# Kernel optimization log

Hardware: AMD Instinct MI355X
Metric: run time of the kernel (lower is better)

## Reference

```python
import jax, jax.numpy as jnp
import numpy as np

N_NODES = 50000
N_EDGES = 50000  # per-node attention scores are used as per-hyperedge weights => M == N
IN_CH = 128
OUT_CH = 128
NNZ = 800000


def setup_inputs() -> dict:
    key = jax.random.key(0)
    k = jax.random.split(key, 7)
    x = jax.random.normal(k[0], (N_NODES, IN_CH), dtype=jnp.float32)
    node_idx = jax.random.randint(k[1], (NNZ,), 0, N_NODES)
    edge_idx = jax.random.randint(k[2], (NNZ,), 0, N_EDGES)
    hyperedge_index = jnp.stack([node_idx, edge_idx]).astype(jnp.int64)
    s_in = 1.0 / np.sqrt(IN_CH)
    attn_w = jax.random.uniform(k[3], (1, IN_CH), minval=-s_in, maxval=s_in, dtype=jnp.float32)
    attn_b = jax.random.uniform(k[4], (1,), minval=-s_in, maxval=s_in, dtype=jnp.float32)
    lin_w = jax.random.uniform(k[5], (OUT_CH, IN_CH), minval=-s_in, maxval=s_in, dtype=jnp.float32)
    bias = jax.random.uniform(k[6], (OUT_CH,), minval=-s_in, maxval=s_in, dtype=jnp.float32)
    return {"x": x, "hyperedge_index": hyperedge_index,
            "attn_w": attn_w, "attn_b": attn_b, "lin_w": lin_w, "bias": bias}


def reference(x, hyperedge_index, attn_w, attn_b, lin_w, bias):
    # x: [N, C_in]; hyperedge_index: [2, nnz] (row 0: node ids, row 1: hyperedge ids)
    node_idx = hyperedge_index[0]
    edge_idx = hyperedge_index[1]
    N = x.shape[0]
    M = N_EDGES

    # edge_weight = sigmoid(attn(x)) -> used as hyperedge_weight (per-edge, M == N)
    w = jax.nn.sigmoid(x @ attn_w.T + attn_b)[:, 0]            # [M]

    xl = x @ lin_w.T                                           # [N, C_out]

    # D_v = sum of incident hyperedge weights per node; D^{-1} with inf -> 0
    D = jax.ops.segment_sum(w[edge_idx], node_idx, num_segments=N)
    Dinv = jnp.where(D > 0, 1.0 / D, 0.0)                      # [N]

    # B_e = hyperedge degree; B^{-1} with inf -> 0
    ones = jnp.ones(edge_idx.shape, dtype=x.dtype)
    Bdeg = jax.ops.segment_sum(ones, edge_idx, num_segments=M)
    Binv = jnp.where(Bdeg > 0, 1.0 / Bdeg, 0.0)                # [M]

    # node -> hyperedge: message = B_e^{-1} * x_j, aggregated at edge e
    msg = Binv[edge_idx][:, None] * xl[node_idx]               # [nnz, C_out]
    e_feat = jax.ops.segment_sum(msg, edge_idx, num_segments=M)

    # hyperedge -> node: message = D_v^{-1} * e_feat, aggregated at node v
    out = jax.ops.segment_sum(e_feat[edge_idx], node_idx, num_segments=N)
    out = Dinv[:, None] * out

    return out + bias
```

## Files before the change

### kernel.cpp

```cpp
#include <hip/hip_runtime.h>
#include <math.h>

#define CH 128
#define CAP 64
#define RSB 9
#define RS  (1 << RSB)
#define CAPB 10240
#define PB 2048

typedef __attribute__((ext_vector_type(8))) short bf16x8;
typedef __attribute__((ext_vector_type(4))) float f32x4;

__device__ __forceinline__ unsigned short f2bf(float f) {
    union { float f; unsigned u; } v; v.f = f;
    unsigned r = v.u + 0x7FFF + ((v.u >> 16) & 1);
    return (unsigned short)(r >> 16);
}
__device__ __forceinline__ float bflo(unsigned u) {
    union { unsigned u; float f; } v; v.u = u << 16; return v.f;
}
__device__ __forceinline__ float bfhi(unsigned u) {
    union { unsigned u; float f; } v; v.u = u & 0xFFFF0000u; return v.f;
}
__device__ __forceinline__ unsigned pack2bf(float a, float b) {
    return (unsigned)f2bf(a) | ((unsigned)f2bf(b) << 16);
}

__global__ __launch_bounds__(256) void fused_main(const float* __restrict__ x,
                                                  const float* __restrict__ attn_w,
                                                  const float* __restrict__ attn_b,
                                                  const float* __restrict__ lw,
                                                  unsigned short* __restrict__ xl,
                                                  float* __restrict__ w,
                                                  int nStrips,
                                                  const int* __restrict__ nidx,
                                                  const int* __restrict__ eidx,
                                                  int* __restrict__ binCnt,
                                                  unsigned int* __restrict__ binData,
                                                  int nnz, int nbd, int SB) {
    __shared__ unsigned short wl[128 * 136];
    __shared__ float awl[128];
    if ((int)blockIdx.x < SB) {
        int* hist = (int*)wl;
        int* base = ((int*)wl) + 256;
        int nbt = 2 * nbd;
        for (int i = threadIdx.x; i < nbt; i += 256) hist[i] = 0;
        __syncthreads();
        int k0 = blockIdx.x * PB + threadIdx.x;
        int vv[8], ee[8], sE[8], sN[8];
#pragma unroll
        for (int u = 0; u < 8; ++u) {
            int k = k0 + u * 256;
            if (k < nnz) {
                int v = nidx[k], e = eidx[k];
                vv[u] = v; ee[u] = e;
                sE[u] = atomicAdd(&hist[e >> RSB], 1);
                sN[u] = atomicAdd(&hist[nbd + (v >> RSB)], 1);
            } else vv[u] = -1;
        }
        __syncthreads();
        for (int i = threadIdx.x; i < nbt; i += 256)
            base[i] = atomicAdd(&binCnt[i], hist[i]);
        __syncthreads();
#pragma unroll
        for (int u = 0; u < 8; ++u) {
            if (vv[u] < 0) continue;
            int bE = ee[u] >> RSB;
            int bN = nbd + (vv[u] >> RSB);
            int iE = min(base[bE] + sE[u], CAPB - 1);
            int iN = min(base[bN] + sN[u], CAPB - 1);
            binData[(size_t)bE * CAPB + iE] = ((unsigned)ee[u] << 16) | (unsigned)vv[u];
            binData[(size_t)bN * CAPB + iN] = ((unsigned)vv[u] << 16) | (unsigned)ee[u];
        }
        return;
    }
    int tid = threadIdx.x;
    for (int i = tid; i < 2048; i += 256) {
        float4 vlo = ((const float4*)lw)[2 * i];
        float4 vhi = ((const float4*)lw)[2 * i + 1];
        int4 dst;
        dst.x = (int)pack2bf(vlo.x, vlo.y);
        dst.y = (int)pack2bf(vlo.z, vlo.w);
        dst.z = (int)pack2bf(vhi.x, vhi.y);
        dst.w = (int)pack2bf(vhi.z, vhi.w);
        *(int4*)(wl + (i >> 4) * 136 + (i & 15) * 8) = dst;
    }
    if (tid < 128) awl[tid] = attn_w[tid];
    float ab = attn_b[0];
    __syncthreads();
    int gb = blockIdx.x - SB;
    int wid = (gb << 2) | (tid >> 6);
    int lane = tid & 63;
    int m = lane & 15, quad = lane >> 4;
    int nWaves = ((int)gridDim.x - SB) << 2;
    for (int s = wid; s < nStrips; s += nWaves) {
        int r0 = s << 4;
        const float* xr = x + (size_t)(r0 + m) * CH + quad * 8;
        float att = 0.f;
        bf16x8 a0, a1, a2, a3;
#define LOAD_FRAG(AFRAG, F)                                                   \
        {                                                                     \
            float4 lo = *(const float4*)(xr + (F) * 32);                      \
            float4 hi = *(const float4*)(xr + (F) * 32 + 4);                  \
            const float* ap = &awl[(F) * 32 + quad * 8];                      \
            att += lo.x * ap[0] + lo.y * ap[1] + lo.z * ap[2] + lo.w * ap[3]  \
                 + hi.x * ap[4] + hi.y * ap[5] + hi.z * ap[6] + hi.w * ap[7]; \
            union { int4 i; bf16x8 v; } pk;                                   \
            pk.i.x = (int)pack2bf(lo.x, lo.y);                                \
            pk.i.y = (int)pack2bf(lo.z, lo.w);                                \
            pk.i.z = (int)pack2bf(hi.x, hi.y);                                \
            pk.i.w = (int)pack2bf(hi.z, hi.w);                                \
            AFRAG = pk.v;                                                     \
        }
        LOAD_FRAG(a0, 0)
        LOAD_FRAG(a1, 1)
        LOAD_FRAG(a2, 2)
        LOAD_FRAG(a3, 3)
#undef LOAD_FRAG
        att += __shfl_xor(att, 16, 64);
        att += __shfl_xor(att, 32, 64);
        if (quad == 0) w[r0 + m] = 1.0f / (1.0f + expf(-(att + ab)));
        unsigned short* orow = xl + (size_t)(r0 + quad * 4) * CH + m;
#pragma unroll
        for (int c0 = 0; c0 < 128; c0 += 16) {
            const unsigned short* wr = wl + (c0 + m) * 136 + quad * 8;
            f32x4 acc = {0.f, 0.f, 0.f, 0.f};
            acc = __builtin_amdgcn_mfma_f32_16x16x32_bf16(a0, *(const bf16x8*)(wr), acc, 0, 0, 0);
            acc = __builtin_amdgcn_mfma_f32_16x16x32_bf16(a1, *(const bf16x8*)(wr + 32), acc, 0, 0, 0);
            acc = __builtin_amdgcn_mfma_f32_16x16x32_bf16(a2, *(const bf16x8*)(wr + 64), acc, 0, 0, 0);
            acc = __builtin_amdgcn_mfma_f32_16x16x32_bf16(a3, *(const bf16x8*)(wr + 96), acc, 0, 0, 0);
            orow[c0]            = f2bf(acc[0]);
            orow[c0 + CH]       = f2bf(acc[1]);
            orow[c0 + 2 * CH]   = f2bf(acc[2]);
            orow[c0 + 3 * CH]   = f2bf(acc[3]);
        }
    }
}

__global__ __launch_bounds__(256) void bucket_build(const int* __restrict__ binCnt,
                                                    const unsigned int* __restrict__ binData,
                                                    int* __restrict__ cntE,
                                                    unsigned short* __restrict__ colE,
                                                    int* __restrict__ cntN,
                                                    unsigned short* __restrict__ colN,
                                                    int nbd, int N) {
    __shared__ int cl[RS];
    int b = blockIdx.x;
    int isN = b >= nbd;
    int bl = isN ? b - nbd : b;
    int idBase = bl << RSB;
    int* cnt = isN ? cntN : cntE;
    unsigned short* col = isN ? colN : colE;
    for (int i = threadIdx.x; i < RS; i += 256) cl[i] = 0;
    __syncthreads();
    int n = min(binCnt[b], CAPB);
    const unsigned int* src = binData + (size_t)b * CAPB;
    for (int i = threadIdx.x; i < n; i += 256) {
        unsigned int entry = src[i];
        int id  = (int)(entry >> 16);
        int val = (int)(entry & 0xFFFFu);
        int r = atomicAdd(&cl[id - idBase], 1);
        col[(size_t)id * CAP + min(r, CAP - 1)] = (unsigned short)val;
    }
    __syncthreads();
    for (int i = threadIdx.x; i < RS; i += 256) {
        int gid = idBase + i;
        if (gid < N) cnt[gid] = cl[i];
    }
}

__global__ __launch_bounds__(256) void edge_pull(const int* __restrict__ cntE,
                                                 const unsigned short* __restrict__ colE,
                                                 const unsigned short* __restrict__ xl,
                                                 unsigned short* __restrict__ ef, int M) {
    int e = (blockIdx.x << 2) | (threadIdx.x >> 6);
    if (e >= M) return;
    int lane = threadIdx.x & 63;
    int deg = cntE[e];
    const unsigned short* col = colE + (size_t)e * CAP;
    float2 a0 = {0.f, 0.f}, a1 = {0.f, 0.f}, a2 = {0.f, 0.f}, a3 = {0.f, 0.f};
    int j = 0;
    for (; j + 3 < deg; j += 4) {
        int v0 = col[j], v1 = col[j + 1], v2 = col[j + 2], v3 = col[j + 3];
        unsigned u0 = *(const unsigned*)(xl + (size_t)v0 * CH + 2 * lane);
        unsigned u1 = *(const unsigned*)(xl + (size_t)v1 * CH + 2 * lane);
        unsigned u2 = *(const unsigned*)(xl + (size_t)v2 * CH + 2 * lane);
        unsigned u3 = *(const unsigned*)(xl + (size_t)v3 * CH + 2 * lane);
        a0.x += bflo(u0); a0.y += bfhi(u0);
        a1.x += bflo(u1); a1.y += bfhi(u1);
        a2.x += bflo(u2); a2.y += bfhi(u2);
        a3.x += bflo(u3); a3.y += bfhi(u3);
    }
    for (; j < deg; ++j) {
        unsigned u0 = *(const unsigned*)(xl + (size_t)col[j] * CH + 2 * lane);
        a0.x += bflo(u0); a0.y += bfhi(u0);
    }
    a0.x += a1.x + a2.x + a3.x;
    a0.y += a1.y + a2.y + a3.y;
    float binv = deg > 0 ? 1.0f / (float)deg : 0.0f;
    *(unsigned*)(ef + (size_t)e * CH + 2 * lane) = pack2bf(a0.x * binv, a0.y * binv);
}

__global__ __launch_bounds__(256) void node_pull(const int* __restrict__ cntN,
                                                 const unsigned short* __restrict__ colN,
                                                 const unsigned short* __restrict__ ef,
                                                 const float* __restrict__ w,
                                                 const float* __restrict__ bias,
                                                 float* __restrict__ out, int N) {
    int v = (blockIdx.x << 2) | (threadIdx.x >> 6);
    if (v >= N) return;
    int lane = threadIdx.x & 63;
    int deg = cntN[v];
    const unsigned short* col = colN + (size_t)v * CAP;
    float2 a0 = {0.f, 0.f}, a1 = {0.f, 0.f}, a2 = {0.f, 0.f}, a3 = {0.f, 0.f};
    float ds = 0.f;
    int j = 0;
    for (; j + 3 < deg; j += 4) {
        int e0 = col[j], e1 = col[j + 1], e2 = col[j + 2], e3 = col[j + 3];
        unsigned u0 = *(const unsigned*)(ef + (size_t)e0 * CH + 2 * lane);
        unsigned u1 = *(const unsigned*)(ef + (size_t)e1 * CH + 2 * lane);
        unsigned u2 = *(const unsigned*)(ef + (size_t)e2 * CH + 2 * lane);
        unsigned u3 = *(const unsigned*)(ef + (size_t)e3 * CH + 2 * lane);
        ds += w[e0] + w[e1] + w[e2] + w[e3];
        a0.x += bflo(u0); a0.y += bfhi(u0);
        a1.x += bflo(u1); a1.y += bfhi(u1);
        a2.x += bflo(u2); a2.y += bfhi(u2);
        a3.x += bflo(u3); a3.y += bfhi(u3);
    }
    for (; j < deg; ++j) {
        int e0 = col[j];
        unsigned u0 = *(const unsigned*)(ef + (size_t)e0 * CH + 2 * lane);
        ds += w[e0];
        a0.x += bflo(u0); a0.y += bfhi(u0);
    }
    a0.x += a1.x + a2.x + a3.x;
    a0.y += a1.y + a2.y + a3.y;
    float dinv = ds > 0.f ? 1.0f / ds : 0.0f;
    float2 bi = *(const float2*)(bias + 2 * lane);
    float2 o = {a0.x * dinv + bi.x, a0.y * dinv + bi.y};
    *(float2*)(out + (size_t)v * CH + 2 * lane) = o;
}

extern "C" void kernel_launch(void* const* d_in, const int* in_sizes, int n_in,
                              void* d_out, int out_size, void* d_ws, size_t ws_size,
                              hipStream_t stream) {
    const float* x      = (const float*)d_in[0];
    const int*   hei    = (const int*)d_in[1];
    const float* attn_w = (const float*)d_in[2];
    const float* attn_b = (const float*)d_in[3];
    const float* lin_w  = (const float*)d_in[4];
    const float* bias   = (const float*)d_in[5];
    float* out = (float*)d_out;

    const int N   = in_sizes[0] / CH;
    const int nnz = in_sizes[1] / 2;
    const int* nidx = hei;
    const int* eidx = hei + nnz;

    unsigned short* S    = (unsigned short*)d_ws;
    float*          w    = (float*)(S + (size_t)N * CH);
    int*            cntE = (int*)(w + N);
    int*            cntN = cntE + N;
    unsigned short* colE = (unsigned short*)(cntN + N);
    unsigned short* colN = colE + (size_t)N * CAP;

    unsigned int* binData = (unsigned int*)S;
    int*          binCnt  = (int*)((char*)d_ws + (size_t)12 * 1024 * 1024);
    unsigned short* efbf = S;
    unsigned short* xlbf = (unsigned short*)out;

    int nbd = (N + RS - 1) >> RSB;
    hipMemsetAsync(binCnt, 0, (size_t)2 * nbd * sizeof(int), stream);

    int SB = (nnz + PB - 1) / PB;
    int nStrips = N / 16;
    int GB = (nStrips + 3) / 4;
    fused_main<<<SB + GB, 256, 0, stream>>>(x, attn_w, attn_b, lin_w, xlbf, w,
                                            nStrips, nidx, eidx, binCnt, binData,
                                            nnz, nbd, SB);

    bucket_build<<<2 * nbd, 256, 0, stream>>>(binCnt, binData, cntE, colE, cntN, colN, nbd, N);
    edge_pull<<<(N + 3) / 4, 256, 0, stream>>>(cntE, colE, xlbf, efbf, N);
    node_pull<<<(N + 3) / 4, 256, 0, stream>>>(cntN, colN, efbf, w, bias, out, N);
}
```

Before: 197.2 us.

## Fuse bucket build into edge and node aggregation kernels via shared-memory buckets

Removes the separate bucket_build kernel and the global colE/colN adjacency arrays. Each aggregation block now rescans one coarse bin's entries, keeps the 64 ids that belong to its sub-range, and builds per-id neighbor lists in shared memory before gathering. This saves one launch and the global write and read-back of the adjacency lists. In exchange each coarse bin is read eight times, once per sub-block, and blocks grow to 512 threads with a 64x64 shared bucket. Bin count atomics are also skipped for empty histogram bins.

```diff
diff --git a/kernel.cpp b/kernel.cpp
--- a/kernel.cpp
+++ b/kernel.cpp
@@ -7,6 +7,8 @@
 #define RS  (1 << RSB)
 #define CAPB 10240
 #define PB 2048
+#define SUB 8
+#define IDS 64
 
 typedef __attribute__((ext_vector_type(8))) short bf16x8;
 typedef __attribute__((ext_vector_type(4))) float f32x4;
@@ -60,7 +62,7 @@
         }
         __syncthreads();
         for (int i = threadIdx.x; i < nbt; i += 256)
-            base[i] = atomicAdd(&binCnt[i], hist[i]);
+            if (hist[i]) base[i] = atomicAdd(&binCnt[i], hist[i]);
         __syncthreads();
 #pragma unroll
         for (int u = 0; u < 8; ++u) {
@@ -137,108 +139,118 @@
     }
 }
 
-__global__ __launch_bounds__(256) void bucket_build(const int* __restrict__ binCnt,
-                                                    const unsigned int* __restrict__ binData,
-                                                    int* __restrict__ cntE,
-                                                    unsigned short* __restrict__ colE,
-                                                    int* __restrict__ cntN,
-                                                    unsigned short* __restrict__ colN,
-                                                    int nbd, int N) {
-    __shared__ int cl[RS];
-    int b = blockIdx.x;
-    int isN = b >= nbd;
-    int bl = isN ? b - nbd : b;
-    int idBase = bl << RSB;
-    int* cnt = isN ? cntN : cntE;
-    unsigned short* col = isN ? colN : colE;
-    for (int i = threadIdx.x; i < RS; i += 256) cl[i] = 0;
-    __syncthreads();
-    int n = min(binCnt[b], CAPB);
-    const unsigned int* src = binData + (size_t)b * CAPB;
-    for (int i = threadIdx.x; i < n; i += 256) {
+__global__ __launch_bounds__(512) void edge_agg(const int* __restrict__ binCnt,
+                                                const unsigned int* __restrict__ binData,
+                                                const unsigned short* __restrict__ xl,
+                                                unsigned short* __restrict__ ef, int M) {
+    __shared__ unsigned short bucket[IDS * CAP];
+    __shared__ int cl[IDS];
+    int cb = blockIdx.x >> 3;
+    int sr = blockIdx.x & (SUB - 1);
+    int idBase = (cb << RSB) + (sr << 6);
+    for (int i = threadIdx.x; i < IDS; i += 512) cl[i] = 0;
+    __syncthreads();
+    int n = min(binCnt[cb], CAPB);
+    const unsigned int* src = binData + (size_t)cb * CAPB;
+    for (int i = threadIdx.x; i < n; i += 512) {
         unsigned int entry = src[i];
-        int id  = (int)(entry >> 16);
-        int val = (int)(entry & 0xFFFFu);
-        int r = atomicAdd(&cl[id - idBase], 1);
-        col[(size_t)id * CAP + min(r, CAP - 1)] = (unsigned short)val;
-    }
-    __syncthreads();
-    for (int i = threadIdx.x; i < RS; i += 256) {
-        int gid = idBase + i;
-        if (gid < N) cnt[gid] = cl[i];
-    }
-}
-
-__global__ __launch_bounds__(256) void edge_pull(const int* __restrict__ cntE,
-                                                 const unsigned short* __restrict__ colE,
-                                                 const unsigned short* __restrict__ xl,
-                                                 unsigned short* __restrict__ ef, int M) {
-    int e = (blockIdx.x << 2) | (threadIdx.x >> 6);
-    if (e >= M) return;
-    int lane = threadIdx.x & 63;
-    int deg = cntE[e];
-    const unsigned short* col = colE + (size_t)e * CAP;
-    float2 a0 = {0.f, 0.f}, a1 = {0.f, 0.f}, a2 = {0.f, 0.f}, a3 = {0.f, 0.f};
-    int j = 0;
-    for (; j + 3 < deg; j += 4) {
-        int v0 = col[j], v1 = col[j + 1], v2 = col[j + 2], v3 = col[j + 3];
-        unsigned u0 = *(const unsigned*)(xl + (size_t)v0 * CH + 2 * lane);
-        unsigned u1 = *(const unsigned*)(xl + (size_t)v1 * CH + 2 * lane);
-        unsigned u2 = *(const unsigned*)(xl + (size_t)v2 * CH + 2 * lane);
-        unsigned u3 = *(const unsigned*)(xl + (size_t)v3 * CH + 2 * lane);
-        a0.x += bflo(u0); a0.y += bfhi(u0);
-        a1.x += bflo(u1); a1.y += bfhi(u1);
-        a2.x += bflo(u2); a2.y += bfhi(u2);
-        a3.x += bflo(u3); a3.y += bfhi(u3);
-    }
-    for (; j < deg; ++j) {
-        unsigned u0 = *(const unsigned*)(xl + (size_t)col[j] * CH + 2 * lane);
-        a0.x += bflo(u0); a0.y += bfhi(u0);
-    }
-    a0.x += a1.x + a2.x + a3.x;
-    a0.y += a1.y + a2.y + a3.y;
-    float binv = deg > 0 ? 1.0f / (float)deg : 0.0f;
-    *(unsigned*)(ef + (size_t)e * CH + 2 * lane) = pack2bf(a0.x * binv, a0.y * binv);
-}
-
-__global__ __launch_bounds__(256) void node_pull(const int* __restrict__ cntN,
-                                                 const unsigned short* __restrict__ colN,
-                                                 const unsigned short* __restrict__ ef,
-                                                 const float* __restrict__ w,
-                                                 const float* __restrict__ bias,
-                                                 float* __restrict__ out, int N) {
-    int v = (blockIdx.x << 2) | (threadIdx.x >> 6);
-    if (v >= N) return;
-    int lane = threadIdx.x & 63;
-    int deg = cntN[v];
-    const unsigned short* col = colN + (size_t)v * CAP;
-    float2 a0 = {0.f, 0.f}, a1 = {0.f, 0.f}, a2 = {0.f, 0.f}, a3 = {0.f, 0.f};
-    float ds = 0.f;
-    int j = 0;
-    for (; j + 3 < deg; j += 4) {
-        int e0 = col[j], e1 = col[j + 1], e2 = col[j + 2], e3 = col[j + 3];
-        unsigned u0 = *(const unsigned*)(ef + (size_t)e0 * CH + 2 * lane);
-        unsigned u1 = *(const unsigned*)(ef + (size_t)e1 * CH + 2 * lane);
-        unsigned u2 = *(const unsigned*)(ef + (size_t)e2 * CH + 2 * lane);
-        unsigned u3 = *(const unsigned*)(ef + (size_t)e3 * CH + 2 * lane);
-        ds += w[e0] + w[e1] + w[e2] + w[e3];
-        a0.x += bflo(u0); a0.y += bfhi(u0);
-        a1.x += bflo(u1); a1.y += bfhi(u1);
-        a2.x += bflo(u2); a2.y += bfhi(u2);
-        a3.x += bflo(u3); a3.y += bfhi(u3);
-    }
-    for (; j < deg; ++j) {
-        int e0 = col[j];
-        unsigned u0 = *(const unsigned*)(ef + (size_t)e0 * CH + 2 * lane);
-        ds += w[e0];
-        a0.x += bflo(u0); a0.y += bfhi(u0);
-    }
-    a0.x += a1.x + a2.x + a3.x;
-    a0.y += a1.y + a2.y + a3.y;
-    float dinv = ds > 0.f ? 1.0f / ds : 0.0f;
-    float2 bi = *(const float2*)(bias + 2 * lane);
-    float2 o = {a0.x * dinv + bi.x, a0.y * dinv + bi.y};
-    *(float2*)(out + (size_t)v * CH + 2 * lane) = o;
+        int lid = (int)(entry >> 16) - idBase;
+        if ((unsigned)lid < IDS) {
+            int r = atomicAdd(&cl[lid], 1);
+            bucket[(lid << 6) + min(r, CAP - 1)] = (unsigned short)(entry & 0xFFFFu);
+        }
+    }
+    __syncthreads();
+    int wid = threadIdx.x >> 6, lane = threadIdx.x & 63;
+    for (int li = wid; li < IDS; li += 8) {
+        int gid = idBase + li;
+        if (gid >= M) break;
+        int deg = cl[li];
+        int dl = min(deg, CAP);
+        const unsigned short* col = bucket + (li << 6);
+        float2 a0 = {0.f, 0.f}, a1 = {0.f, 0.f}, a2 = {0.f, 0.f}, a3 = {0.f, 0.f};
+        int j = 0;
+        for (; j + 3 < dl; j += 4) {
+            int v0 = col[j], v1 = col[j + 1], v2 = col[j + 2], v3 = col[j + 3];
+            unsigned u0 = *(const unsigned*)(xl + (size_t)v0 * CH + 2 * lane);
+            unsigned u1 = *(const unsigned*)(xl + (size_t)v1 * CH + 2 * lane);
+            unsigned u2 = *(const unsigned*)(xl + (size_t)v2 * CH + 2 * lane);
+            unsigned u3 = *(const unsigned*)(xl + (size_t)v3 * CH + 2 * lane);
+            a0.x += bflo(u0); a0.y += bfhi(u0);
+            a1.x += bflo(u1); a1.y += bfhi(u1);
+            a2.x += bflo(u2); a2.y += bfhi(u2);
+            a3.x += bflo(u3); a3.y += bfhi(u3);
+        }
+        for (; j < dl; ++j) {
+            unsigned u0 = *(const unsigned*)(xl + (size_t)col[j] * CH + 2 * lane);
+            a0.x += bflo(u0); a0.y += bfhi(u0);
+        }
+        a0.x += a1.x + a2.x + a3.x;
+        a0.y += a1.y + a2.y + a3.y;
+        float binv = deg > 0 ? 1.0f / (float)deg : 0.0f;
+        *(unsigned*)(ef + (size_t)gid * CH + 2 * lane) = pack2bf(a0.x * binv, a0.y * binv);
+    }
+}
+
+__global__ __launch_bounds__(512) void node_agg(const int* __restrict__ binCnt,
+                                                const unsigned int* __restrict__ binData,
+                                                const unsigned short* __restrict__ ef,
+                                                const float* __restrict__ w,
+                                                const float* __restrict__ bias,
+                                                float* __restrict__ out, int N) {
+    __shared__ unsigned short bucket[IDS * CAP];
+    __shared__ int cl[IDS];
+    int cb = blockIdx.x >> 3;
+    int sr = blockIdx.x & (SUB - 1);
+    int idBase = (cb << RSB) + (sr << 6);
+    for (int i = threadIdx.x; i < IDS; i += 512) cl[i] = 0;
+    __syncthreads();
+    int n = min(binCnt[cb], CAPB);
+    const unsigned int* src = binData + (size_t)cb * CAPB;
+    for (int i = threadIdx.x; i < n; i += 512) {
+        unsigned int entry = src[i];
+        int lid = (int)(entry >> 16) - idBase;
+        if ((unsigned)lid < IDS) {
+            int r = atomicAdd(&cl[lid], 1);
+            bucket[(lid << 6) + min(r, CAP - 1)] = (unsigned short)(entry & 0xFFFFu);
+        }
+    }
+    __syncthreads();
+    int wid = threadIdx.x >> 6, lane = threadIdx.x & 63;
+    for (int li = wid; li < IDS; li += 8) {
+        int gid = idBase + li;
+        if (gid >= N) break;
+        int deg = cl[li];
+        int dl = min(deg, CAP);
+        const unsigned short* col = bucket + (li << 6);
+        float2 a0 = {0.f, 0.f}, a1 = {0.f, 0.f}, a2 = {0.f, 0.f}, a3 = {0.f, 0.f};
+        float ds = 0.f;
+        int j = 0;
+        for (; j + 3 < dl; j += 4) {
+            int e0 = col[j], e1 = col[j + 1], e2 = col[j + 2], e3 = col[j + 3];
+            unsigned u0 = *(const unsigned*)(ef + (size_t)e0 * CH + 2 * lane);
+            unsigned u1 = *(const unsigned*)(ef + (size_t)e1 * CH + 2 * lane);
+            unsigned u2 = *(const unsigned*)(ef + (size_t)e2 * CH + 2 * lane);
+            unsigned u3 = *(const unsigned*)(ef + (size_t)e3 * CH + 2 * lane);
+            ds += w[e0] + w[e1] + w[e2] + w[e3];
+            a0.x += bflo(u0); a0.y += bfhi(u0);
+            a1.x += bflo(u1); a1.y += bfhi(u1);
+            a2.x += bflo(u2); a2.y += bfhi(u2);
+            a3.x += bflo(u3); a3.y += bfhi(u3);
+        }
+        for (; j < dl; ++j) {
+            int e0 = col[j];
+            unsigned u0 = *(const unsigned*)(ef + (size_t)e0 * CH + 2 * lane);
+            ds += w[e0];
+            a0.x += bflo(u0); a0.y += bfhi(u0);
+        }
+        a0.x += a1.x + a2.x + a3.x;
+        a0.y += a1.y + a2.y + a3.y;
+        float dinv = ds > 0.f ? 1.0f / ds : 0.0f;
+        float2 bi = *(const float2*)(bias + 2 * lane);
+        float2 o = {a0.x * dinv + bi.x, a0.y * dinv + bi.y};
+        *(float2*)(out + (size_t)gid * CH + 2 * lane) = o;
+    }
 }
 
 extern "C" void kernel_launch(void* const* d_in, const int* in_sizes, int n_in,
@@ -257,19 +269,14 @@
     const int* nidx = hei;
     const int* eidx = hei + nnz;
 
-    unsigned short* S    = (unsigned short*)d_ws;
-    float*          w    = (float*)(S + (size_t)N * CH);
-    int*            cntE = (int*)(w + N);
-    int*            cntN = cntE + N;
-    unsigned short* colE = (unsigned short*)(cntN + N);
-    unsigned short* colN = colE + (size_t)N * CAP;
-
-    unsigned int* binData = (unsigned int*)S;
-    int*          binCnt  = (int*)((char*)d_ws + (size_t)12 * 1024 * 1024);
-    unsigned short* efbf = S;
+    unsigned short* efbf = (unsigned short*)d_ws;
+    float*          w    = (float*)(efbf + (size_t)N * CH);
+    unsigned int*   binData = (unsigned int*)(w + N);
+    int nbd = (N + RS - 1) >> RSB;
+    int*            binCnt  = (int*)(binData + (size_t)2 * nbd * CAPB);
+
     unsigned short* xlbf = (unsigned short*)out;
 
-    int nbd = (N + RS - 1) >> RSB;
     hipMemsetAsync(binCnt, 0, (size_t)2 * nbd * sizeof(int), stream);
 
     int SB = (nnz + PB - 1) / PB;
@@ -279,7 +286,8 @@
                                             nStrips, nidx, eidx, binCnt, binData,
                                             nnz, nbd, SB);
 
-    bucket_build<<<2 * nbd, 256, 0, stream>>>(binCnt, binData, cntE, colE, cntN, colN, nbd, N);
-    edge_pull<<<(N + 3) / 4, 256, 0, stream>>>(cntE, colE, xlbf, efbf, N);
-    node_pull<<<(N + 3) / 4, 256, 0, stream>>>(cntN, colN, efbf, w, bias, out, N);
-}
+    edge_agg<<<nbd * SUB, 512, 0, stream>>>(binCnt, binData, xlbf, efbf, N);
+    node_agg<<<nbd * SUB, 512, 0, stream>>>(binCnt + nbd,
+                                            binData + (size_t)nbd * CAPB,
+                                            efbf, w, bias, out, N);
+}
```

Result: faster. 180.3 us (-8.6%).
